# Optimization experiments

Measured on AMD Instinct MI355X. Metric: run time of the kernel, lower is better.

The kernel has to match this reference:

```python
import jax, jax.numpy as jnp
import numpy as np

B, S, d, D = 128, 1024, 64, 64  # batch, seq_len, physical dim, bond dim


def setup_inputs() -> dict:
    key = jax.random.key(0)
    k1, k2, k3, k4 = jax.random.split(key, 4)
    k_core = (d * D * D) ** (-0.5)
    k_vec = d ** (-0.5)
    core = k_core * jax.random.normal(k1, (d, D, D), dtype=jnp.float32)
    left_boundary = k_vec * jax.random.normal(k2, (D,), dtype=jnp.float32)
    right_boundary = k_vec * jax.random.normal(k3, (D,), dtype=jnp.float32)
    X = jax.random.randint(k4, (B, S), 0, d, dtype=jnp.int32)
    return {"X": X, "core": core, "left_boundary": left_boundary,
            "right_boundary": right_boundary}


def reference(X, core, left_boundary, right_boundary):
    """Faithful JAX version of TTrain._log_contract_at_batch (homogeneous).

    X: [B, S] int category indices; core: [d, D, D]; boundaries: [D].
    Returns logprobs: [B].
    The per-step normalization (infinity-norm) + accumulated log-norm trick of
    the original is preserved exactly; the final
    log((exp(lognorm) * out)**2) is computed in the mathematically identical
    stable form 2*(lognorm + log|out|).
    """
    batch = X.shape[0]
    lb = jnp.broadcast_to(left_boundary, (batch, left_boundary.shape[0]))  # [B, D]
    Z0 = jnp.max(jnp.abs(lb), axis=1)                                      # [B]
    c0 = lb / Z0[:, None]
    logn0 = jnp.log(Z0)

    def step(carry, x_t):
        c, logn = carry                       # c: [B, D]
        w_t = core[x_t]                       # gather selected cores: [B, D, D]
        ct = jnp.einsum('bi,bij->bj', c, w_t)  # [B, D]
        Zt = jnp.max(jnp.abs(ct), axis=1)      # [B] infinity norm
        return (ct / Zt[:, None], logn + jnp.log(Zt)), None

    (c, logn), _ = jax.lax.scan(step, (c0, logn0), X.T)  # scan over seq axis
    out = jnp.einsum('bi,i->b', c, right_boundary)        # [B]
    logprobs = 2.0 * (logn + jnp.log(jnp.abs(out)))
    return logprobs
```

## Files before the change

kernel.cpp:

```cpp
#include <hip/hip_runtime.h>
#include <math.h>


#define TT_S 1024
#define TT_D 64
#define NCHUNK 16
#define CLEN 64

typedef __attribute__((ext_vector_type(8))) short short8;
typedef __attribute__((ext_vector_type(4))) float float4v;
typedef __attribute__((ext_vector_type(4))) unsigned uint4v;
typedef __attribute__((ext_vector_type(2))) unsigned uint2v;

static __device__ __forceinline__ short8 as_short8(uint4v u) {
    union { uint4v u; short8 s; } x; x.u = u; return x.s;
}

static __device__ __forceinline__ short bf16_rne(float f) {
    unsigned u = __float_as_uint(f);
    return (short)((u + 0x7FFFu + ((u >> 16) & 1u)) >> 16);
}

__global__ __launch_bounds__(256) void tt_prep(
    const float* __restrict__ core, short* __restrict__ tblA,
    short* __restrict__ tblBt)
{
    const int x = blockIdx.x;
    const int l = threadIdx.x & 63, r = threadIdx.x >> 6;
    const int n = l & 15, q = l >> 4;
    const float* W = core + x * 4096;

    if (r < 2) {
        #pragma unroll
        for (int Ii = 0; Ii < 2; ++Ii) {
            const int I = 2 * r + Ii;
            #pragma unroll
            for (int Kp = 0; Kp < 2; ++Kp) {
                short8 v;
                const int row = 16 * I + n;
                const int c0 = 32 * Kp + 4 * q;
                #pragma unroll
                for (int j = 0; j < 8; ++j) {
                    const int col = c0 + 16 * (j >> 2) + (j & 3);
                    v[j] = bf16_rne(W[row * 64 + col]);
                }
                *(short8*)(tblA + ((size_t)(x * 8 + I * 2 + Kp) * 64 + l) * 8) = v;
            }
        }
    } else {
        const int Kp = r - 2;
        #pragma unroll
        for (int J = 0; J < 4; ++J) {
            short8 v;
            const int col = 16 * J + n;
            const int r0 = 32 * Kp + 4 * q;
            #pragma unroll
            for (int j = 0; j < 8; ++j) {
                const int row = r0 + 16 * (j >> 2) + (j & 3);
                v[j] = bf16_rne(W[row * 64 + col]);
            }
            *(short8*)(tblBt + ((size_t)(x * 8 + Kp * 4 + J) * 64 + l) * 8) = v;
        }
    }
}

__global__ __launch_bounds__(64, 2) void tt_stage1(
    const int* __restrict__ X, const short* __restrict__ tblA,
    const short* __restrict__ tblBt, short* __restrict__ PT,
    float* __restrict__ ln1)
{
    {
        const int ph = blockIdx.x & 3;
        if (ph > 0) __builtin_amdgcn_s_sleep(9);
        if (ph > 1) __builtin_amdgcn_s_sleep(9);
        if (ph > 2) __builtin_amdgcn_s_sleep(9);
    }

    const int w = blockIdx.x;
    const int b = w >> 4, chunk = w & 15;
    const int l = threadIdx.x, n = l & 15, q = l >> 4;

    const int xv = X[b * TT_S + chunk * CLEN + l];
    #define XT(t) __builtin_amdgcn_readlane(xv, (t))

    const float4v zero = {0.f, 0.f, 0.f, 0.f};
    float4v acc[4][4];
    short8 A0[8], A1[8];
    float logn = 0.f;

    #define PK(hi, lo) __builtin_amdgcn_perm(__float_as_uint(hi),             \
                                             __float_as_uint(lo), 0x07060302u)

    #define LOAD_FRAGS(DST, TBL, XIDX)                                        \
    {   const short8* p_ = (const short8*)((TBL) + (size_t)(XIDX) * 4096) + l; \
        _Pragma("unroll")                                                     \
        for (int f_ = 0; f_ < 8; ++f_) (DST)[f_] = p_[f_ * 64]; }

    #define MFMA_TBL(ABUF, BBUF)                                              \
        _Pragma("unroll")                                                     \
        for (int I_ = 0; I_ < 4; ++I_)                                        \
            _Pragma("unroll")                                                 \
            for (int J_ = 0; J_ < 4; ++J_) {                                  \
                float4v c0_ = __builtin_amdgcn_mfma_f32_16x16x32_bf16(        \
                    (ABUF)[2 * I_ + 0], (BBUF)[J_], zero, 0, 0, 0);           \
                acc[I_][J_] = __builtin_amdgcn_mfma_f32_16x16x32_bf16(        \
                    (ABUF)[2 * I_ + 1], (BBUF)[4 + J_], c0_, 0, 0, 0);        \
            }

    #define PROD(ABUF)                                                        \
        _Pragma("unroll")                                                     \
        for (int J_ = 0; J_ < 4; ++J_) {                                      \
            uint4v u0_, u1_;                                                  \
            u0_[0] = PK(acc[0][J_][1], acc[0][J_][0]);                        \
            u0_[1] = PK(acc[0][J_][3], acc[0][J_][2]);                        \
            u0_[2] = PK(acc[1][J_][1], acc[1][J_][0]);                        \
            u0_[3] = PK(acc[1][J_][3], acc[1][J_][2]);                        \
            u1_[0] = PK(acc[2][J_][1], acc[2][J_][0]);                        \
            u1_[1] = PK(acc[2][J_][3], acc[2][J_][2]);                        \
            u1_[2] = PK(acc[3][J_][1], acc[3][J_][0]);                        \
            u1_[3] = PK(acc[3][J_][3], acc[3][J_][2]);                        \
            const short8 bl_ = as_short8(u0_);                                \
            const short8 bh_ = as_short8(u1_);                                \
            _Pragma("unroll")                                                 \
            for (int I_ = 0; I_ < 4; ++I_) {                                  \
                float4v c0_ = __builtin_amdgcn_mfma_f32_16x16x32_bf16(        \
                    (ABUF)[2 * I_ + 0], bl_, zero, 0, 0, 0);                  \
                acc[I_][J_] = __builtin_amdgcn_mfma_f32_16x16x32_bf16(        \
                    (ABUF)[2 * I_ + 1], bh_, c0_, 0, 0, 0);                   \
            }                                                                 \
        }

    #define RENORM()                                                          \
    {   float Z_ = 0.f;                                                       \
        _Pragma("unroll")                                                     \
        for (int I_ = 0; I_ < 4; ++I_)                                        \
            _Pragma("unroll")                                                 \
            for (int J_ = 0; J_ < 4; ++J_)                                    \
                _Pragma("unroll")                                             \
                for (int r_ = 0; r_ < 4; ++r_)                                \
                    Z_ = fmaxf(Z_, fabsf(acc[I_][J_][r_]));                   \
        _Pragma("unroll")                                                     \
        for (int m_ = 32; m_; m_ >>= 1) Z_ = fmaxf(Z_, __shfl_xor(Z_, m_));   \
        logn += logf(Z_);                                                     \
        const float rZ_ = 1.0f / Z_;                                          \
        _Pragma("unroll")                                                     \
        for (int I_ = 0; I_ < 4; ++I_)                                        \
            _Pragma("unroll")                                                 \
            for (int J_ = 0; J_ < 4; ++J_)                                    \
                _Pragma("unroll")                                             \
                for (int r_ = 0; r_ < 4; ++r_) acc[I_][J_][r_] *= rZ_; }

    {
        short8 Bt[8];
        LOAD_FRAGS(Bt, tblBt, XT(CLEN - 1))
        LOAD_FRAGS(A0, tblA, XT(CLEN - 2))
        LOAD_FRAGS(A1, tblA, XT(CLEN - 3))
        MFMA_TBL(A0, Bt)
    }
    LOAD_FRAGS(A0, tblA, XT(CLEN - 4))

    #pragma unroll 1
    for (int it = 0; it < 31; ++it) {
        PROD(A1)
        {
            const int tn = 59 - 2 * it;
            LOAD_FRAGS(A1, tblA, XT(tn < 0 ? 0 : tn))
        }
        if (((2 * it + 2) & 7) == 0) RENORM()
        PROD(A0)
        {
            const int tn = 58 - 2 * it;
            LOAD_FRAGS(A0, tblA, XT(tn < 0 ? 0 : tn))
        }
    }

    {
        float Z = 0.f;
        #pragma unroll
        for (int I = 0; I < 4; ++I)
            #pragma unroll
            for (int J = 0; J < 4; ++J)
                #pragma unroll
                for (int r = 0; r < 4; ++r) Z = fmaxf(Z, fabsf(acc[I][J][r]));
        #pragma unroll
        for (int m = 32; m; m >>= 1) Z = fmaxf(Z, __shfl_xor(Z, m));
        logn += logf(Z);
        const float rZ = 1.0f / Z;
        short* base = PT + (size_t)w * 4096;
        #pragma unroll
        for (int I = 0; I < 4; ++I)
            #pragma unroll
            for (int J = 0; J < 4; ++J) {
                float4v v = acc[I][J];
                #pragma unroll
                for (int r = 0; r < 4; ++r) v[r] *= rZ;
                uint2v dd;
                dd[0] = PK(v[1], v[0]);
                dd[1] = PK(v[3], v[2]);
                *(uint2v*)(base + (16 * J + n) * 64 + 16 * I + 4 * q) = dd;
            }
        if (l == 0) ln1[w] = logn;
    }
    #undef LOAD_FRAGS
    #undef MFMA_TBL
    #undef PROD
    #undef RENORM
    #undef PK
    #undef XT
}

__global__ __launch_bounds__(64, 1) void tt_stage2(
    const short* __restrict__ PT, const float* __restrict__ ln1,
    const float* __restrict__ lb, const float* __restrict__ rb,
    float* __restrict__ out)
{
    __shared__ float cb[64];
    const int b = blockIdx.x, j = threadIdx.x;

    float c = lb[j];
    float Z = fabsf(c);
    #pragma unroll
    for (int m = 32; m; m >>= 1) Z = fmaxf(Z, __shfl_xor(Z, m));
    float logn = logf(Z);
    c *= (1.0f / Z);

    float ln = (j < NCHUNK) ? ln1[b * NCHUNK + j] : 0.f;
    #pragma unroll
    for (int m = 32; m; m >>= 1) ln += __shfl_xor(ln, m);
    logn += ln;

    const short* base = PT + (size_t)b * NCHUNK * 4096 + j * 64;

    short8 bufA[8], bufB[8];
    #pragma unroll
    for (int f = 0; f < 8; ++f) bufA[f] = ((const short8*)base)[f];

    #define S2_STEP(BUF)                                                      \
    {                                                                         \
        cb[j] = c;                                                            \
        asm volatile("s_waitcnt lgkmcnt(0)" ::: "memory");                    \
        float a0 = 0.f, a1 = 0.f, a2 = 0.f, a3 = 0.f;                         \
        _Pragma("unroll")                                                     \
        for (int f = 0; f < 8; ++f) {                                         \
            union { short8 s; uint4v u; } uu; uu.s = (BUF)[f];                \
            const float4v cv0 = *(const float4v*)(cb + 8 * f);                \
            const float4v cv1 = *(const float4v*)(cb + 8 * f + 4);            \
            a0 = fmaf(cv0[0], __uint_as_float(uu.u[0] << 16), a0);            \
            a1 = fmaf(cv0[1], __uint_as_float(uu.u[0] & 0xffff0000u), a1);    \
            a2 = fmaf(cv0[2], __uint_as_float(uu.u[1] << 16), a2);            \
            a3 = fmaf(cv0[3], __uint_as_float(uu.u[1] & 0xffff0000u), a3);    \
            a0 = fmaf(cv1[0], __uint_as_float(uu.u[2] << 16), a0);            \
            a1 = fmaf(cv1[1], __uint_as_float(uu.u[2] & 0xffff0000u), a1);    \
            a2 = fmaf(cv1[2], __uint_as_float(uu.u[3] << 16), a2);            \
            a3 = fmaf(cv1[3], __uint_as_float(uu.u[3] & 0xffff0000u), a3);    \
        }                                                                     \
        float cn = (a0 + a1) + (a2 + a3);                                     \
        float Zl = fabsf(cn);                                                 \
        _Pragma("unroll")                                                     \
        for (int m = 32; m; m >>= 1) Zl = fmaxf(Zl, __shfl_xor(Zl, m));       \
        logn += logf(Zl);                                                     \
        c = cn * (1.0f / Zl);                                                 \
    }

    #pragma unroll 1
    for (int k = 0; k < NCHUNK; k += 2) {
        {   const short8* p = (const short8*)(base + (size_t)(k + 1) * 4096);
            #pragma unroll
            for (int f = 0; f < 8; ++f) bufB[f] = p[f];
        }
        asm volatile("" ::: "memory");
        S2_STEP(bufA)
        {   const int kn = (k + 2 < NCHUNK) ? (k + 2) : (NCHUNK - 1);
            const short8* p = (const short8*)(base + (size_t)kn * 4096);
            #pragma unroll
            for (int f = 0; f < 8; ++f) bufA[f] = p[f];
        }
        asm volatile("" ::: "memory");
        S2_STEP(bufB)
    }
    #undef S2_STEP

    float dot = c * rb[j];
    #pragma unroll
    for (int m = 32; m; m >>= 1) dot += __shfl_xor(dot, m);
    if (j == 0) out[b] = 2.0f * (logn + logf(fabsf(dot)));
}

__global__ __launch_bounds__(256) void tt_transpose(
    const float* __restrict__ core, float* __restrict__ coreT)
{
    __shared__ float tile[64][65];
    const int x = blockIdx.x;
    const float* src = core + x * 4096;
    float* dst = coreT + x * 4096;
    const int r0 = threadIdx.x >> 6, cc = threadIdx.x & 63;
    #pragma unroll
    for (int k = 0; k < 16; ++k) tile[r0 + 4 * k][cc] = src[(r0 + 4 * k) * 64 + cc];
    __syncthreads();
    #pragma unroll
    for (int k = 0; k < 16; ++k) dst[(r0 + 4 * k) * 64 + cc] = tile[cc][r0 + 4 * k];
}

__global__ __launch_bounds__(64, 1) void ttrain_chain2(
    const int* __restrict__ X, const float* __restrict__ coreT,
    const float* __restrict__ lb, const float* __restrict__ rb,
    float* __restrict__ out)
{
    __shared__ float cbuf[2][64];
    const int b = blockIdx.x, j = threadIdx.x;
    const int* Xrow = X + b * TT_S;
    float c = lb[j];
    float Z = fabsf(c);
    #pragma unroll
    for (int m = 32; m; m >>= 1) Z = fmaxf(Z, __shfl_xor(Z, m));
    float logn = logf(Z);
    c *= (1.0f / Z);
    const float* colbase = coreT + j * 64;
    int xs_cur = Xrow[j];
    int xs_nxt = Xrow[64 + j];
    float4 wA[16], wB[16];
    {
        const int x0 = Xrow[0];
        const float4* p = (const float4*)(colbase + x0 * 4096);
        #pragma unroll
        for (int k = 0; k < 16; ++k) wA[k] = p[k];
    }
    #define TT_STEP(WCUR, WNXT, SLOT, XNEXT, T)                              \
    {                                                                        \
        cbuf[SLOT][j] = c;                                                   \
        {                                                                    \
            const float4* pre = (const float4*)(colbase + (XNEXT) * 4096);   \
            _Pragma("unroll")                                                \
            for (int k = 0; k < 16; ++k) WNXT[k] = pre[k];                   \
        }                                                                    \
        asm volatile("s_waitcnt lgkmcnt(0)" ::: "memory");                   \
        float a0 = 0.f, a1 = 0.f, a2 = 0.f, a3 = 0.f;                        \
        const float4* cb2 = (const float4*)cbuf[SLOT];                       \
        _Pragma("unroll")                                                    \
        for (int k = 0; k < 16; ++k) {                                       \
            float4 cv = cb2[k];                                              \
            a0 = fmaf(cv.x, WCUR[k].x, a0);                                  \
            a1 = fmaf(cv.y, WCUR[k].y, a1);                                  \
            a2 = fmaf(cv.z, WCUR[k].z, a2);                                  \
            a3 = fmaf(cv.w, WCUR[k].w, a3);                                  \
        }                                                                    \
        float cn = (a0 + a1) + (a2 + a3);                                    \
        if (((T) & 7) == 7) {                                                \
            float Zl = fabsf(cn);                                            \
            _Pragma("unroll")                                                \
            for (int m = 32; m; m >>= 1) Zl = fmaxf(Zl, __shfl_xor(Zl, m));  \
            logn += logf(Zl);                                                \
            cn *= (1.0f / Zl);                                               \
        }                                                                    \
        c = cn;                                                              \
    }
    for (int tc = 0; tc < TT_S; tc += 64) {
        #pragma unroll 1
        for (int u = 0; u < 64; u += 2) {
            const int x1 = __builtin_amdgcn_readlane(xs_cur, u + 1);
            TT_STEP(wA, wB, 0, x1, tc + u)
            const int src2 = (u + 2 < 64) ? xs_cur : xs_nxt;
            const int x2 = __builtin_amdgcn_readlane(src2, (u + 2) & 63);
            TT_STEP(wB, wA, 1, x2, tc + u + 1)
        }
        xs_cur = xs_nxt;
        const int nc = tc + 128;
        xs_nxt = Xrow[((nc < TT_S) ? nc : 0) + j];
    }
    #undef TT_STEP
    float dot = c * rb[j];
    #pragma unroll
    for (int m = 32; m; m >>= 1) dot += __shfl_xor(dot, m);
    if (j == 0) out[b] = 2.0f * (logn + logf(fabsf(dot)));
}

extern "C" void kernel_launch(void* const* d_in, const int* in_sizes, int n_in,
                              void* d_out, int out_size, void* d_ws, size_t ws_size,
                              hipStream_t stream) {
    const int*   X    = (const int*)d_in[0];
    const float* core = (const float*)d_in[1];
    const float* lb   = (const float*)d_in[2];
    const float* rb   = (const float*)d_in[3];
    float* out = (float*)d_out;

    const int B = in_sizes[0] / TT_S;
    const size_t tblBytes = (size_t)64 * 8 * 64 * 8 * sizeof(short);
    const size_t ptBytes  = (size_t)B * NCHUNK * 4096 * sizeof(short);
    const size_t lnBytes  = (size_t)B * NCHUNK * sizeof(float);
    const size_t need = 2 * tblBytes + ptBytes + lnBytes;

    if (ws_size >= need) {
        char* w = (char*)d_ws;
        short* tblA  = (short*)w;
        short* tblBt = (short*)(w + tblBytes);
        short* PT    = (short*)(w + 2 * tblBytes);
        float* ln1   = (float*)(w + 2 * tblBytes + ptBytes);
        tt_prep<<<64, 256, 0, stream>>>(core, tblA, tblBt);
        tt_stage1<<<B * NCHUNK, 64, 0, stream>>>(X, tblA, tblBt, PT, ln1);
        tt_stage2<<<B, 64, 0, stream>>>(PT, ln1, lb, rb, out);
    } else if (ws_size >= (size_t)64 * 4096 * sizeof(float)) {
        float* coreT = (float*)d_ws;
        tt_transpose<<<64, 256, 0, stream>>>(core, coreT);
        ttrain_chain2<<<B, TT_D, 0, stream>>>(X, coreT, lb, rb, out);
    }
}
```

Measured before the change: 132.4 us.

## Precompute pairwise core products to halve the sequential chain length

Adds a kernel that builds a table of all 64x64 pairs of core-matrix products, each rounded to bf16 in MFMA fragment layout. A new stage-1 kernel then walks each 64-token chunk with one lookup per two tokens, so the serial MFMA dependency chain is half as long, with renormalisation adjusted to match. The cost is a 32 MB table built on every call plus an extra bf16 rounding of each product. The s_sleep staggering at kernel start is dropped, and the fp32 fallback for small workspaces is removed.

New measurement: 156.9 us. +18.6%, slower.

```diff
diff --git a/kernel.cpp b/kernel.cpp
--- a/kernel.cpp
+++ b/kernel.cpp
@@ -64,115 +64,152 @@
     }
 }
 
-__global__ __launch_bounds__(64, 2) void tt_stage1(
+#define PK(hi, lo) __builtin_amdgcn_perm(__float_as_uint(hi),                 \
+                                         __float_as_uint(lo), 0x07060302u)
+
+#define LOAD_FRAGS(DST, TBL, XIDX)                                            \
+{   const short8* p_ = (const short8*)((TBL) + (size_t)(XIDX) * 4096) + l;    \
+    _Pragma("unroll")                                                         \
+    for (int f_ = 0; f_ < 8; ++f_) (DST)[f_] = p_[f_ * 64]; }
+
+#define MFMA_TBL(ACC, ABUF, BBUF)                                             \
+    _Pragma("unroll")                                                         \
+    for (int I_ = 0; I_ < 4; ++I_)                                            \
+        _Pragma("unroll")                                                     \
+        for (int J_ = 0; J_ < 4; ++J_) {                                      \
+            float4v c0_ = __builtin_amdgcn_mfma_f32_16x16x32_bf16(            \
+                (ABUF)[2 * I_ + 0], (BBUF)[J_], zero, 0, 0, 0);               \
+            (ACC)[I_][J_] = __builtin_amdgcn_mfma_f32_16x16x32_bf16(          \
+                (ABUF)[2 * I_ + 1], (BBUF)[4 + J_], c0_, 0, 0, 0);            \
+        }
+
+#define PROD(ACC, ABUF)                                                       \
+    _Pragma("unroll")                                                         \
+    for (int J_ = 0; J_ < 4; ++J_) {                                          \
+        uint4v u0_, u1_;                                                      \
+        u0_[0] = PK((ACC)[0][J_][1], (ACC)[0][J_][0]);                        \
+        u0_[1] = PK((ACC)[0][J_][3], (ACC)[0][J_][2]);                        \
+        u0_[2] = PK((ACC)[1][J_][1], (ACC)[1][J_][0]);                        \
+        u0_[3] = PK((ACC)[1][J_][3], (ACC)[1][J_][2]);                        \
+        u1_[0] = PK((ACC)[2][J_][1], (ACC)[2][J_][0]);                        \
+        u1_[1] = PK((ACC)[2][J_][3], (ACC)[2][J_][2]);                        \
+        u1_[2] = PK((ACC)[3][J_][1], (ACC)[3][J_][0]);                        \
+        u1_[3] = PK((ACC)[3][J_][3], (ACC)[3][J_][2]);                        \
+        const short8 bl_ = as_short8(u0_);                                    \
+        const short8 bh_ = as_short8(u1_);                                    \
+        _Pragma("unroll")                                                     \
+        for (int I_ = 0; I_ < 4; ++I_) {                                      \
+            float4v c0_ = __builtin_amdgcn_mfma_f32_16x16x32_bf16(            \
+                (ABUF)[2 * I_ + 0], bl_, zero, 0, 0, 0);                      \
+            (ACC)[I_][J_] = __builtin_amdgcn_mfma_f32_16x16x32_bf16(          \
+                (ABUF)[2 * I_ + 1], bh_, c0_, 0, 0, 0);                       \
+        }                                                                     \
+    }
+
+#define RENORM(ACC, LOGN)                                                     \
+{   float Z_ = 0.f;                                                           \
+    _Pragma("unroll")                                                         \
+    for (int I_ = 0; I_ < 4; ++I_)                                            \
+        _Pragma("unroll")                                                     \
+        for (int J_ = 0; J_ < 4; ++J_)                                        \
+            _Pragma("unroll")                                                 \
+            for (int r_ = 0; r_ < 4; ++r_)                                    \
+                Z_ = fmaxf(Z_, fabsf((ACC)[I_][J_][r_]));                     \
+    _Pragma("unroll")                                                         \
+    for (int m_ = 32; m_; m_ >>= 1) Z_ = fmaxf(Z_, __shfl_xor(Z_, m_));       \
+    (LOGN) += logf(Z_);                                                       \
+    const float rZ_ = 1.0f / Z_;                                              \
+    _Pragma("unroll")                                                         \
+    for (int I_ = 0; I_ < 4; ++I_)                                            \
+        _Pragma("unroll")                                                     \
+        for (int J_ = 0; J_ < 4; ++J_)                                        \
+            _Pragma("unroll")                                                 \
+            for (int r_ = 0; r_ < 4; ++r_) (ACC)[I_][J_][r_] *= rZ_; }
+
+__global__ __launch_bounds__(64, 2) void tt_prep_pair(
+    const short* __restrict__ tblA, const short* __restrict__ tblBt,
+    short* __restrict__ tblP)
+{
+    __shared__ short mt[64 * 68];
+    const int pi = blockIdx.x >> 6, pj = blockIdx.x & 63;
+    const int l = threadIdx.x, n = l & 15, q = l >> 4;
+
+    const float4v zero = {0.f, 0.f, 0.f, 0.f};
+    float4v acc[4][4];
+    short8 Af[8], Bf[8];
+    LOAD_FRAGS(Af, tblA, pi)
+    LOAD_FRAGS(Bf, tblBt, pj)
+    MFMA_TBL(acc, Af, Bf)
+
+    #pragma unroll
+    for (int I = 0; I < 4; ++I)
+        #pragma unroll
+        for (int J = 0; J < 4; ++J) {
+            const float4v v = acc[I][J];
+            uint2v dd;
+            dd[0] = ((unsigned)(unsigned short)bf16_rne(v[0])) |
+                    (((unsigned)(unsigned short)bf16_rne(v[1])) << 16);
+            dd[1] = ((unsigned)(unsigned short)bf16_rne(v[2])) |
+                    (((unsigned)(unsigned short)bf16_rne(v[3])) << 16);
+            *(uint2v*)(mt + (16 * J + n) * 68 + 16 * I + 4 * q) = dd;
+        }
+    asm volatile("s_waitcnt lgkmcnt(0)" ::: "memory");
+
+    #pragma unroll
+    for (int f = 0; f < 8; ++f) {
+        const int I = f >> 1, Kp = f & 1;
+        short8 v;
+        #pragma unroll
+        for (int j = 0; j < 8; ++j) {
+            const int c = 32 * Kp + 4 * q + 16 * (j >> 2) + (j & 3);
+            v[j] = mt[c * 68 + 16 * I + n];
+        }
+        *(short8*)(tblP + (size_t)blockIdx.x * 4096 + (size_t)(f * 64 + l) * 8) = v;
+    }
+}
+
+__global__ __launch_bounds__(64, 2) void tt_stage1p(
     const int* __restrict__ X, const short* __restrict__ tblA,
-    const short* __restrict__ tblBt, short* __restrict__ PT,
-    float* __restrict__ ln1)
+    const short* __restrict__ tblBt, const short* __restrict__ tblP,
+    short* __restrict__ PT, float* __restrict__ ln1)
 {
-    {
-        const int ph = blockIdx.x & 3;
-        if (ph > 0) __builtin_amdgcn_s_sleep(9);
-        if (ph > 1) __builtin_amdgcn_s_sleep(9);
-        if (ph > 2) __builtin_amdgcn_s_sleep(9);
-    }
-
     const int w = blockIdx.x;
     const int b = w >> 4, chunk = w & 15;
     const int l = threadIdx.x, n = l & 15, q = l >> 4;
 
     const int xv = X[b * TT_S + chunk * CLEN + l];
     #define XT(t) __builtin_amdgcn_readlane(xv, (t))
+    #define PIDX(k) (XT(2 * (k)) * 64 + XT(2 * (k) + 1))
 
     const float4v zero = {0.f, 0.f, 0.f, 0.f};
     float4v acc[4][4];
     short8 A0[8], A1[8];
     float logn = 0.f;
 
-    #define PK(hi, lo) __builtin_amdgcn_perm(__float_as_uint(hi),             \
-                                             __float_as_uint(lo), 0x07060302u)
-
-    #define LOAD_FRAGS(DST, TBL, XIDX)                                        \
-    {   const short8* p_ = (const short8*)((TBL) + (size_t)(XIDX) * 4096) + l; \
-        _Pragma("unroll")                                                     \
-        for (int f_ = 0; f_ < 8; ++f_) (DST)[f_] = p_[f_ * 64]; }
-
-    #define MFMA_TBL(ABUF, BBUF)                                              \
-        _Pragma("unroll")                                                     \
-        for (int I_ = 0; I_ < 4; ++I_)                                        \
-            _Pragma("unroll")                                                 \
-            for (int J_ = 0; J_ < 4; ++J_) {                                  \
-                float4v c0_ = __builtin_amdgcn_mfma_f32_16x16x32_bf16(        \
-                    (ABUF)[2 * I_ + 0], (BBUF)[J_], zero, 0, 0, 0);           \
-                acc[I_][J_] = __builtin_amdgcn_mfma_f32_16x16x32_bf16(        \
-                    (ABUF)[2 * I_ + 1], (BBUF)[4 + J_], c0_, 0, 0, 0);        \
-            }
-
-    #define PROD(ABUF)                                                        \
-        _Pragma("unroll")                                                     \
-        for (int J_ = 0; J_ < 4; ++J_) {                                      \
-            uint4v u0_, u1_;                                                  \
-            u0_[0] = PK(acc[0][J_][1], acc[0][J_][0]);                        \
-            u0_[1] = PK(acc[0][J_][3], acc[0][J_][2]);                        \
-            u0_[2] = PK(acc[1][J_][1], acc[1][J_][0]);                        \
-            u0_[3] = PK(acc[1][J_][3], acc[1][J_][2]);                        \
-            u1_[0] = PK(acc[2][J_][1], acc[2][J_][0]);                        \
-            u1_[1] = PK(acc[2][J_][3], acc[2][J_][2]);                        \
-            u1_[2] = PK(acc[3][J_][1], acc[3][J_][0]);                        \
-            u1_[3] = PK(acc[3][J_][3], acc[3][J_][2]);                        \
-            const short8 bl_ = as_short8(u0_);                                \
-            const short8 bh_ = as_short8(u1_);                                \
-            _Pragma("unroll")                                                 \
-            for (int I_ = 0; I_ < 4; ++I_) {                                  \
-                float4v c0_ = __builtin_amdgcn_mfma_f32_16x16x32_bf16(        \
-                    (ABUF)[2 * I_ + 0], bl_, zero, 0, 0, 0);                  \
-                acc[I_][J_] = __builtin_amdgcn_mfma_f32_16x16x32_bf16(        \
-                    (ABUF)[2 * I_ + 1], bh_, c0_, 0, 0, 0);                   \
-            }                                                                 \
-        }
-
-    #define RENORM()                                                          \
-    {   float Z_ = 0.f;                                                       \
-        _Pragma("unroll")                                                     \
-        for (int I_ = 0; I_ < 4; ++I_)                                        \
-            _Pragma("unroll")                                                 \
-            for (int J_ = 0; J_ < 4; ++J_)                                    \
-                _Pragma("unroll")                                             \
-                for (int r_ = 0; r_ < 4; ++r_)                                \
-                    Z_ = fmaxf(Z_, fabsf(acc[I_][J_][r_]));                   \
-        _Pragma("unroll")                                                     \
-        for (int m_ = 32; m_; m_ >>= 1) Z_ = fmaxf(Z_, __shfl_xor(Z_, m_));   \
-        logn += logf(Z_);                                                     \
-        const float rZ_ = 1.0f / Z_;                                          \
-        _Pragma("unroll")                                                     \
-        for (int I_ = 0; I_ < 4; ++I_)                                        \
-            _Pragma("unroll")                                                 \
-            for (int J_ = 0; J_ < 4; ++J_)                                    \
-                _Pragma("unroll")                                             \
-                for (int r_ = 0; r_ < 4; ++r_) acc[I_][J_][r_] *= rZ_; }
-
     {
         short8 Bt[8];
         LOAD_FRAGS(Bt, tblBt, XT(CLEN - 1))
         LOAD_FRAGS(A0, tblA, XT(CLEN - 2))
-        LOAD_FRAGS(A1, tblA, XT(CLEN - 3))
-        MFMA_TBL(A0, Bt)
-    }
-    LOAD_FRAGS(A0, tblA, XT(CLEN - 4))
+        LOAD_FRAGS(A1, tblP, PIDX(30))
+        MFMA_TBL(acc, A0, Bt)
+    }
+    LOAD_FRAGS(A0, tblP, PIDX(29))
 
     #pragma unroll 1
-    for (int it = 0; it < 31; ++it) {
-        PROD(A1)
+    for (int it = 0; it < 15; ++it) {
+        if (it & 1) RENORM(acc, logn)
+        PROD(acc, A1)
         {
-            const int tn = 59 - 2 * it;
-            LOAD_FRAGS(A1, tblA, XT(tn < 0 ? 0 : tn))
-        }
-        if (((2 * it + 2) & 7) == 0) RENORM()
-        PROD(A0)
+            const int kn = 28 - 2 * it;
+            LOAD_FRAGS(A1, tblP, PIDX(kn < 0 ? 0 : kn))
+        }
+        PROD(acc, A0)
         {
-            const int tn = 58 - 2 * it;
-            LOAD_FRAGS(A0, tblA, XT(tn < 0 ? 0 : tn))
-        }
-    }
+            const int kn = 27 - 2 * it;
+            LOAD_FRAGS(A0, tblP, PIDX(kn < 0 ? 0 : kn))
+        }
+    }
+    PROD(acc, A1)
 
     {
         float Z = 0.f;
@@ -201,11 +238,78 @@
             }
         if (l == 0) ln1[w] = logn;
     }
-    #undef LOAD_FRAGS
-    #undef MFMA_TBL
-    #undef PROD
-    #undef RENORM
-    #undef PK
+    #undef XT
+    #undef PIDX
+}
+
+__global__ __launch_bounds__(64, 2) void tt_stage1(
+    const int* __restrict__ X, const short* __restrict__ tblA,
+    const short* __restrict__ tblBt, short* __restrict__ PT,
+    float* __restrict__ ln1)
+{
+    const int w = blockIdx.x;
+    const int b = w >> 4, chunk = w & 15;
+    const int l = threadIdx.x, n = l & 15, q = l >> 4;
+
+    const int xv = X[b * TT_S + chunk * CLEN + l];
+    #define XT(t) __builtin_amdgcn_readlane(xv, (t))
+
+    const float4v zero = {0.f, 0.f, 0.f, 0.f};
+    float4v acc[4][4];
+    short8 A0[8], A1[8];
+    float logn = 0.f;
+
+    {
+        short8 Bt[8];
+        LOAD_FRAGS(Bt, tblBt, XT(CLEN - 1))
+        LOAD_FRAGS(A0, tblA, XT(CLEN - 2))
+        LOAD_FRAGS(A1, tblA, XT(CLEN - 3))
+        MFMA_TBL(acc, A0, Bt)
+    }
+    LOAD_FRAGS(A0, tblA, XT(CLEN - 4))
+
+    #pragma unroll 1
+    for (int it = 0; it < 31; ++it) {
+        PROD(acc, A1)
+        {
+            const int tn = 59 - 2 * it;
+            LOAD_FRAGS(A1, tblA, XT(tn < 0 ? 0 : tn))
+        }
+        if (((2 * it + 2) & 7) == 0) RENORM(acc, logn)
+        PROD(acc, A0)
+        {
+            const int tn = 58 - 2 * it;
+            LOAD_FRAGS(A0, tblA, XT(tn < 0 ? 0 : tn))
+        }
+    }
+
+    {
+        float Z = 0.f;
+        #pragma unroll
+        for (int I = 0; I < 4; ++I)
+            #pragma unroll
+            for (int J = 0; J < 4; ++J)
+                #pragma unroll
+                for (int r = 0; r < 4; ++r) Z = fmaxf(Z, fabsf(acc[I][J][r]));
+        #pragma unroll
+        for (int m = 32; m; m >>= 1) Z = fmaxf(Z, __shfl_xor(Z, m));
+        logn += logf(Z);
+        const float rZ = 1.0f / Z;
+        short* base = PT + (size_t)w * 4096;
+        #pragma unroll
+        for (int I = 0; I < 4; ++I)
+            #pragma unroll
+            for (int J = 0; J < 4; ++J) {
+                float4v v = acc[I][J];
+                #pragma unroll
+                for (int r = 0; r < 4; ++r) v[r] *= rZ;
+                uint2v dd;
+                dd[0] = PK(v[1], v[0]);
+                dd[1] = PK(v[3], v[2]);
+                *(uint2v*)(base + (16 * J + n) * 64 + 16 * I + 4 * q) = dd;
+            }
+        if (l == 0) ln1[w] = logn;
+    }
     #undef XT
 }
 
@@ -286,94 +390,6 @@
     if (j == 0) out[b] = 2.0f * (logn + logf(fabsf(dot)));
 }
 
-__global__ __launch_bounds__(256) void tt_transpose(
-    const float* __restrict__ core, float* __restrict__ coreT)
-{
-    __shared__ float tile[64][65];
-    const int x = blockIdx.x;
-    const float* src = core + x * 4096;
-    float* dst = coreT + x * 4096;
-    const int r0 = threadIdx.x >> 6, cc = threadIdx.x & 63;
-    #pragma unroll
-    for (int k = 0; k < 16; ++k) tile[r0 + 4 * k][cc] = src[(r0 + 4 * k) * 64 + cc];
-    __syncthreads();
-    #pragma unroll
-    for (int k = 0; k < 16; ++k) dst[(r0 + 4 * k) * 64 + cc] = tile[cc][r0 + 4 * k];
-}
-
-__global__ __launch_bounds__(64, 1) void ttrain_chain2(
-    const int* __restrict__ X, const float* __restrict__ coreT,
-    const float* __restrict__ lb, const float* __restrict__ rb,
-    float* __restrict__ out)
-{
-    __shared__ float cbuf[2][64];
-    const int b = blockIdx.x, j = threadIdx.x;
-    const int* Xrow = X + b * TT_S;
-    float c = lb[j];
-    float Z = fabsf(c);
-    #pragma unroll
-    for (int m = 32; m; m >>= 1) Z = fmaxf(Z, __shfl_xor(Z, m));
-    float logn = logf(Z);
-    c *= (1.0f / Z);
-    const float* colbase = coreT + j * 64;
-    int xs_cur = Xrow[j];
-    int xs_nxt = Xrow[64 + j];
-    float4 wA[16], wB[16];
-    {
-        const int x0 = Xrow[0];
-        const float4* p = (const float4*)(colbase + x0 * 4096);
-        #pragma unroll
-        for (int k = 0; k < 16; ++k) wA[k] = p[k];
-    }
-    #define TT_STEP(WCUR, WNXT, SLOT, XNEXT, T)                              \
-    {                                                                        \
-        cbuf[SLOT][j] = c;                                                   \
-        {                                                                    \
-            const float4* pre = (const float4*)(colbase + (XNEXT) * 4096);   \
-            _Pragma("unroll")                                                \
-            for (int k = 0; k < 16; ++k) WNXT[k] = pre[k];                   \
-        }                                                                    \
-        asm volatile("s_waitcnt lgkmcnt(0)" ::: "memory");                   \
-        float a0 = 0.f, a1 = 0.f, a2 = 0.f, a3 = 0.f;                        \
-        const float4* cb2 = (const float4*)cbuf[SLOT];                       \
-        _Pragma("unroll")                                                    \
-        for (int k = 0; k < 16; ++k) {                                       \
-            float4 cv = cb2[k];                                              \
-            a0 = fmaf(cv.x, WCUR[k].x, a0);                                  \
-            a1 = fmaf(cv.y, WCUR[k].y, a1);                                  \
-            a2 = fmaf(cv.z, WCUR[k].z, a2);                                  \
-            a3 = fmaf(cv.w, WCUR[k].w, a3);                                  \
-        }                                                                    \
-        float cn = (a0 + a1) + (a2 + a3);                                    \
-        if (((T) & 7) == 7) {                                                \
-            float Zl = fabsf(cn);                                            \
-            _Pragma("unroll")                                                \
-            for (int m = 32; m; m >>= 1) Zl = fmaxf(Zl, __shfl_xor(Zl, m));  \
-            logn += logf(Zl);                                                \
-            cn *= (1.0f / Zl);                                               \
-        }                                                                    \
-        c = cn;                                                              \
-    }
-    for (int tc = 0; tc < TT_S; tc += 64) {
-        #pragma unroll 1
-        for (int u = 0; u < 64; u += 2) {
-            const int x1 = __builtin_amdgcn_readlane(xs_cur, u + 1);
-            TT_STEP(wA, wB, 0, x1, tc + u)
-            const int src2 = (u + 2 < 64) ? xs_cur : xs_nxt;
-            const int x2 = __builtin_amdgcn_readlane(src2, (u + 2) & 63);
-            TT_STEP(wB, wA, 1, x2, tc + u + 1)
-        }
-        xs_cur = xs_nxt;
-        const int nc = tc + 128;
-        xs_nxt = Xrow[((nc < TT_S) ? nc : 0) + j];
-    }
-    #undef TT_STEP
-    float dot = c * rb[j];
-    #pragma unroll
-    for (int m = 32; m; m >>= 1) dot += __shfl_xor(dot, m);
-    if (j == 0) out[b] = 2.0f * (logn + logf(fabsf(dot)));
-}
-
 extern "C" void kernel_launch(void* const* d_in, const int* in_sizes, int n_in,
                               void* d_out, int out_size, void* d_ws, size_t ws_size,
                               hipStream_t stream) {
@@ -384,23 +400,30 @@
     float* out = (float*)d_out;
 
     const int B = in_sizes[0] / TT_S;
-    const size_t tblBytes = (size_t)64 * 8 * 64 * 8 * sizeof(short);
-    const size_t ptBytes  = (size_t)B * NCHUNK * 4096 * sizeof(short);
-    const size_t lnBytes  = (size_t)B * NCHUNK * sizeof(float);
-    const size_t need = 2 * tblBytes + ptBytes + lnBytes;
-
-    if (ws_size >= need) {
-        char* w = (char*)d_ws;
-        short* tblA  = (short*)w;
-        short* tblBt = (short*)(w + tblBytes);
-        short* PT    = (short*)(w + 2 * tblBytes);
-        float* ln1   = (float*)(w + 2 * tblBytes + ptBytes);
+    const size_t tblBytes  = (size_t)64 * 8 * 64 * 8 * sizeof(short);
+    const size_t pairBytes = (size_t)4096 * 4096 * sizeof(short);
+    const size_t ptBytes   = (size_t)B * NCHUNK * 4096 * sizeof(short);
+    const size_t lnBytes   = (size_t)B * NCHUNK * sizeof(float);
+    const size_t needPair  = 2 * tblBytes + pairBytes + ptBytes + lnBytes;
+    const size_t needBase  = 2 * tblBytes + ptBytes + lnBytes;
+
+    char* w = (char*)d_ws;
+    short* tblA  = (short*)w;
+    short* tblBt = (short*)(w + tblBytes);
+
+    if (ws_size >= needPair) {
+        short* tblP = (short*)(w + 2 * tblBytes);
+        short* PT   = (short*)(w + 2 * tblBytes + pairBytes);
+        float* ln1  = (float*)(w + 2 * tblBytes + pairBytes + ptBytes);
+        tt_prep<<<64, 256, 0, stream>>>(core, tblA, tblBt);
+        tt_prep_pair<<<4096, 64, 0, stream>>>(tblA, tblBt, tblP);
+        tt_stage1p<<<B * NCHUNK, 64, 0, stream>>>(X, tblA, tblBt, tblP, PT, ln1);
+        tt_stage2<<<B, 64, 0, stream>>>(PT, ln1, lb, rb, out);
+    } else if (ws_size >= needBase) {
+        short* PT  = (short*)(w + 2 * tblBytes);
+        float* ln1 = (float*)(w + 2 * tblBytes + ptBytes);
         tt_prep<<<64, 256, 0, stream>>>(core, tblA, tblBt);
         tt_stage1<<<B * NCHUNK, 64, 0, stream>>>(X, tblA, tblBt, PT, ln1);
         tt_stage2<<<B, 64, 0, stream>>>(PT, ln1, lb, rb, out);
-    } else if (ws_size >= (size_t)64 * 4096 * sizeof(float)) {
-        float* coreT = (float*)d_ws;
-        tt_transpose<<<64, 256, 0, stream>>>(core, coreT);
-        ttrain_chain2<<<B, TT_D, 0, stream>>>(X, coreT, lb, rb, out);
-    }
-}
+    }
+}
```
